# Optimization experiments

Hardware: AMD Instinct MI355X
Metric: run time of the kernel (lower is better)

## Reference

```python
import jax, jax.numpy as jnp
import numpy as np

NUM_EXPERTS = 64
TOP_K = 2
B, S, EMB, MLP = 4, 2048, 1024, 2048


def setup_inputs() -> dict:
    key = jax.random.key(0)
    k1, k2, k3, k4, k5 = jax.random.split(key, 5)
    inputs = jax.random.normal(k1, (B, S, EMB), dtype=jnp.float32)
    gate_kernel = jax.random.normal(k2, (EMB, NUM_EXPERTS), dtype=jnp.float32) / np.sqrt(EMB)
    w0 = jax.random.normal(k3, (NUM_EXPERTS, EMB, MLP), dtype=jnp.float32) / np.sqrt(EMB)
    w1 = jax.random.normal(k4, (NUM_EXPERTS, EMB, MLP), dtype=jnp.float32) / np.sqrt(EMB)
    wo = jax.random.normal(k5, (NUM_EXPERTS, MLP, EMB), dtype=jnp.float32) / np.sqrt(MLP)
    return {"inputs": inputs, "gate_kernel": gate_kernel, "w0": w0, "w1": w1, "wo": wo}


def reference(inputs, gate_kernel, w0, w1, wo):
    b, s, e = inputs.shape
    x = inputs.reshape(b * s, e)                                  # [T, E]
    # Router (DenseGeneral gate)
    gate_logits = jnp.einsum('te,ex->tx', x, gate_kernel)         # [T, X]
    # permute(): top-k gating + sort tokens by expert
    weights, selected = jax.lax.top_k(gate_logits, TOP_K)         # [T, K]
    weights = jax.nn.softmax(weights.astype(jnp.float32), axis=-1)
    flat_experts = selected.reshape(-1)                           # [T*K]
    sort_idx = jnp.argsort(flat_experts)                          # [T*K]
    token_idx = sort_idx // TOP_K
    sorted_x = jnp.take(x, token_idx, axis=0)                     # [T*K, E]
    group_sizes = jnp.bincount(flat_experts, length=NUM_EXPERTS).astype(jnp.int32)
    # grouped GEMMs (gated FFN: silu(x@w0) * (x@w1) @ wo)
    h0 = jax.lax.ragged_dot(sorted_x, w0, group_sizes)            # [T*K, M]
    h1 = jax.lax.ragged_dot(sorted_x, w1, group_sizes)            # [T*K, M]
    inter = jax.nn.silu(h0) * h1
    out_sorted = jax.lax.ragged_dot(inter, wo, group_sizes)       # [T*K, E]
    # unpermute(): restore token order, weighted combine over top-k
    unsorted = jnp.take(out_sorted, jnp.argsort(sort_idx), axis=0)
    per_tok = unsorted.reshape(b * s, TOP_K, e)
    out = jnp.einsum('BKE,BK->BE', per_tok.astype(jnp.float32), weights)
    return out.reshape(b, s, e)
```

## Files before the change

### kernel.cpp

```cpp
#include <hip/hip_runtime.h>
#include <hip/hip_bf16.h>
#include <math.h>

#define NTOK   8192
#define NEXP   64
#define EMBD   1024
#define MLPD   2048
#define TOPK   2
#define NFLAT  (NTOK * TOPK)
#define BKD    32
#define MAXCH  8

typedef __attribute__((ext_vector_type(4)))  float  f32x4;
typedef __attribute__((ext_vector_type(2)))  float  f32x2;
typedef __attribute__((ext_vector_type(16))) float  f32x16;
typedef __attribute__((ext_vector_type(8)))  __bf16 bf16x8;
typedef __attribute__((ext_vector_type(4)))  __bf16 bf16x4;

__device__ __forceinline__ void gl16(const void* g, void* lds_base) {
  __builtin_amdgcn_global_load_lds(
      (const __attribute__((address_space(1))) unsigned int*)g,
      (__attribute__((address_space(3))) unsigned int*)lds_base, 16, 0, 0);
}

#define OFF_COUNTS 0
#define OFF_BASE   256
#define OFF_RUN    512
#define OFF_EFLAT  1024
#define OFF_WFLAT  (1024 + 65536)
#define OFF_ROWTOK (1024 + 2 * 65536)
#define OFF_F2R    (1024 + 3 * 65536)
#define OFF_INTER  (1024 + 4 * 65536)
#define OFF_OS     (OFF_INTER + (size_t)NFLAT * MLPD * 2)
#define OFF_XB     OFF_OS
#define NEED_F32   (OFF_OS + (size_t)NFLAT * EMBD * 4)

__global__ __launch_bounds__(256) void cvt_x_k(const float* __restrict__ x,
                                               __bf16* __restrict__ xb) {
  size_t i = ((size_t)blockIdx.x * 256 + threadIdx.x) * 8;
  f32x4 f0 = *(const f32x4*)(x + i);
  f32x4 f1 = *(const f32x4*)(x + i + 4);
  bf16x8 v;
  #pragma unroll
  for (int q = 0; q < 4; ++q) { v[q] = (__bf16)f0[q]; v[4 + q] = (__bf16)f1[q]; }
  *(bf16x8*)(xb + i) = v;
}

__global__ __launch_bounds__(256) void router_topk(
    const float* __restrict__ x, const float* __restrict__ gk,
    int* __restrict__ e_flat, float* __restrict__ w_flat) {
  int t = blockIdx.x * 4 + (threadIdx.x >> 6);
  int l = threadIdx.x & 63;
  const float* xr = x + (size_t)t * EMBD;
  float acc = 0.f;
  #pragma unroll 8
  for (int i = 0; i < EMBD; ++i)
    acc = fmaf(xr[i], gk[i * NEXP + l], acc);
  float m = acc;
  for (int o = 32; o; o >>= 1) m = fmaxf(m, __shfl_xor(m, o));
  unsigned long long b1 = __ballot(acc == m);
  int i1 = __ffsll(b1) - 1;
  float v2 = (l == i1) ? -INFINITY : acc;
  float m2 = v2;
  for (int o = 32; o; o >>= 1) m2 = fmaxf(m2, __shfl_xor(m2, o));
  unsigned long long b2 = __ballot(v2 == m2);
  int i2 = __ffsll(b2) - 1;
  if (l == 0) {
    float e2 = expf(m2 - m);
    float inv = 1.f / (1.f + e2);
    e_flat[2 * t] = i1;  e_flat[2 * t + 1] = i2;
    w_flat[2 * t] = inv; w_flat[2 * t + 1] = e2 * inv;
  }
}

__global__ void hist_k(const int* __restrict__ ef, int* __restrict__ counts) {
  int j = blockIdx.x * 256 + threadIdx.x;
  if (j < NFLAT) atomicAdd(&counts[ef[j]], 1);
}

__global__ void scan_k(const int* __restrict__ counts, int* __restrict__ base) {
  if (threadIdx.x == 0) {
    int s = 0;
    for (int e = 0; e < NEXP; ++e) { base[e] = s; s += counts[e]; }
  }
}

__global__ void scatter_k(const int* __restrict__ ef, const int* __restrict__ base,
                          int* __restrict__ run, int* __restrict__ rowtok,
                          int* __restrict__ f2r) {
  int j = blockIdx.x * 256 + threadIdx.x;
  if (j < NFLAT) {
    int e = ef[j];
    int r = base[e] + atomicAdd(&run[e], 1);
    f2r[j] = r;
    rowtok[r] = j >> 1;
  }
}

__global__ __launch_bounds__(256, 3) void gemm1_k(
    const __bf16* __restrict__ xb, const float* __restrict__ w0,
    const float* __restrict__ w1, const int* __restrict__ counts,
    const int* __restrict__ base, const int* __restrict__ rowtok,
    __hip_bfloat16* __restrict__ inter) {
  int e = blockIdx.z;
  int Me = counts[e];
  int mc = blockIdx.y;
  if (mc * 128 >= Me) return;
  int rs = base[e];
  int nb = blockIdx.x * 64;
  int t = threadIdx.x;
  int wv = t >> 6, l = t & 63;
  int wr = wv >> 1, wc = wv & 1;
  int lo = l & 31, hi = l >> 5;

  __shared__ __bf16 Ax[3][4096];
  __shared__ __bf16 Bx[3][4096];

  int rga = mc * 128 + wv * 32 + lo; rga = rga < Me ? rga : Me - 1;
  const __bf16* abase = xb + (size_t)rowtok[rs + rga] * EMBD + hi * 8;
  int bm = t >> 7, ko = (t >> 5) & 3, np = t & 31;
  const float* bgb = (bm ? w1 : w0) + (size_t)e * EMBD * MLPD + nb + np * 2;
  int n0 = np * 2;
  int bslot = ((bm * 2 + (ko >> 1)) * 2 + (n0 >> 5)) * 64 + (ko & 1) * 32 + (n0 & 31);

  f32x2 vb[8];

  auto LOADB = [&](int ks) {
    int kk = ks * BKD;
    #pragma unroll
    for (int j = 0; j < 8; ++j)
      vb[j] = *(const f32x2*)(bgb + (size_t)(kk + ko * 8 + j) * MLPD);
  };
  auto WRITEB = [&](int buf) {
    bf16x8 c0, c1;
    #pragma unroll
    for (int j = 0; j < 8; ++j) { c0[j] = (__bf16)vb[j][0]; c1[j] = (__bf16)vb[j][1]; }
    *(bf16x8*)&Bx[buf][bslot * 8]     = c0;
    *(bf16x8*)&Bx[buf][bslot * 8 + 8] = c1;
  };
  auto STAGEA = [&](int ks, int buf) {
    int kk = ks * BKD;
    #pragma unroll
    for (int kh = 0; kh < 2; ++kh)
      gl16(abase + kk + kh * 16, &Ax[buf][(wv * 2 + kh) * 512]);
  };

  f32x16 acc0[2], acc1[2];
  #pragma unroll
  for (int g = 0; g < 2; ++g)
    #pragma unroll
    for (int r = 0; r < 16; ++r) { acc0[g][r] = 0.f; acc1[g][r] = 0.f; }

  const int NT = EMBD / BKD;
  LOADB(0);
  asm volatile("s_waitcnt vmcnt(0)" ::: "memory");
  WRITEB(0);
  LOADB(1);
  __builtin_amdgcn_sched_barrier(0);
  STAGEA(0, 0);
  STAGEA(1, 1);

  for (int ks = 0; ks < NT; ++ks) {
    int cur = ks % 3;
    if (ks + 1 < NT) asm volatile("s_waitcnt vmcnt(2)" ::: "memory");
    else             asm volatile("s_waitcnt vmcnt(0)" ::: "memory");
    __builtin_amdgcn_sched_barrier(0);
    asm volatile("s_waitcnt lgkmcnt(0)" ::: "memory");
    __builtin_amdgcn_sched_barrier(0);
    __builtin_amdgcn_s_barrier();
    if (ks + 1 < NT) WRITEB((ks + 1) % 3);
    __builtin_amdgcn_sched_barrier(0);
    if (ks + 2 < NT) LOADB(ks + 2);
    __builtin_amdgcn_sched_barrier(0);
    if (ks + 2 < NT) STAGEA(ks + 2, (ks + 2) % 3);
    __builtin_amdgcn_sched_barrier(0);

    bf16x8 av[2][2], bv0[2], bv1[2];
    #pragma unroll
    for (int g = 0; g < 2; ++g)
      #pragma unroll
      for (int kh = 0; kh < 2; ++kh)
        av[g][kh] = *(const bf16x8*)&Ax[cur][((wr * 2 + g) * 2 + kh) * 512 + l * 8];
    #pragma unroll
    for (int kh = 0; kh < 2; ++kh) {
      bv0[kh] = *(const bf16x8*)&Bx[cur][((0 + kh) * 2 + wc) * 512 + l * 8];
      bv1[kh] = *(const bf16x8*)&Bx[cur][((2 + kh) * 2 + wc) * 512 + l * 8];
    }
    #pragma unroll
    for (int kh = 0; kh < 2; ++kh)
      #pragma unroll
      for (int g = 0; g < 2; ++g) {
        acc0[g] = __builtin_amdgcn_mfma_f32_32x32x16_bf16(av[g][kh], bv0[kh], acc0[g], 0, 0, 0);
        acc1[g] = __builtin_amdgcn_mfma_f32_32x32x16_bf16(av[g][kh], bv1[kh], acc1[g], 0, 0, 0);
      }
  }

  #pragma unroll
  for (int g = 0; g < 2; ++g)
    #pragma unroll
    for (int r = 0; r < 16; ++r) {
      int rl = mc * 128 + wr * 64 + g * 32 + (r & 3) + 8 * (r >> 2) + 4 * hi;
      if (rl < Me) {
        float h0 = acc0[g][r], h1 = acc1[g][r];
        float s = h0 / (1.f + expf(-h0)) * h1;
        inter[(size_t)(rs + rl) * MLPD + nb + wc * 32 + lo] = (__hip_bfloat16)s;
      }
    }
}

template <typename OS_T>
__global__ __launch_bounds__(256, 4) void gemm2_k(
    const __hip_bfloat16* __restrict__ inter, const float* __restrict__ wo,
    const int* __restrict__ counts, const int* __restrict__ base,
    OS_T* __restrict__ os) {
  int e = blockIdx.z;
  int Me = counts[e];
  int mc = blockIdx.y;
  if (mc * 128 >= Me) return;
  int rs = base[e];
  int nb = blockIdx.x * 64;
  int t = threadIdx.x;
  int wv = t >> 6, l = t & 63;
  int wr = wv >> 1, wc = wv & 1;
  int lo = l & 31, hi = l >> 5;

  __shared__ __bf16 Ax[3][4096];
  __shared__ __bf16 Bx[3][2048];

  int rga = mc * 128 + wv * 32 + lo; rga = rga < Me ? rga : Me - 1;
  const __bf16* abase = (const __bf16*)inter + (size_t)(rs + rga) * MLPD + hi * 8;
  int kq = t >> 5, np = t & 31;
  const float* bgb = wo + (size_t)e * MLPD * EMBD + nb + np * 2;
  int n0 = np * 2;
  int bslot = ((kq >> 2) * 2 + (n0 >> 5)) * 64 + ((kq >> 1) & 1) * 32 + (n0 & 31);
  int qo = (kq & 1) * 4;

  f32x2 vb[4];

  auto LOADB = [&](int ks) {
    int kk = ks * BKD;
    #pragma unroll
    for (int j = 0; j < 4; ++j)
      vb[j] = *(const f32x2*)(bgb + (size_t)(kk + kq * 4 + j) * EMBD);
  };
  auto WRITEB = [&](int buf) {
    bf16x4 c0, c1;
    #pragma unroll
    for (int j = 0; j < 4; ++j) { c0[j] = (__bf16)vb[j][0]; c1[j] = (__bf16)vb[j][1]; }
    *(bf16x4*)&Bx[buf][bslot * 8 + qo]     = c0;
    *(bf16x4*)&Bx[buf][bslot * 8 + 8 + qo] = c1;
  };
  auto STAGEA = [&](int ks, int buf) {
    int kk = ks * BKD;
    #pragma unroll
    for (int kh = 0; kh < 2; ++kh)
      gl16(abase + kk + kh * 16, &Ax[buf][(wv * 2 + kh) * 512]);
  };

  f32x16 acc[2];
  #pragma unroll
  for (int g = 0; g < 2; ++g)
    #pragma unroll
    for (int r = 0; r < 16; ++r) acc[g][r] = 0.f;

  const int NT = MLPD / BKD;
  LOADB(0);
  asm volatile("s_waitcnt vmcnt(0)" ::: "memory");
  WRITEB(0);
  LOADB(1);
  __builtin_amdgcn_sched_barrier(0);
  STAGEA(0, 0);
  STAGEA(1, 1);

  for (int ks = 0; ks < NT; ++ks) {
    int cur = ks % 3;
    if (ks + 1 < NT) asm volatile("s_waitcnt vmcnt(2)" ::: "memory");
    else             asm volatile("s_waitcnt vmcnt(0)" ::: "memory");
    __builtin_amdgcn_sched_barrier(0);
    asm volatile("s_waitcnt lgkmcnt(0)" ::: "memory");
    __builtin_amdgcn_sched_barrier(0);
    __builtin_amdgcn_s_barrier();
    if (ks + 1 < NT) WRITEB((ks + 1) % 3);
    __builtin_amdgcn_sched_barrier(0);
    if (ks + 2 < NT) LOADB(ks + 2);
    __builtin_amdgcn_sched_barrier(0);
    if (ks + 2 < NT) STAGEA(ks + 2, (ks + 2) % 3);
    __builtin_amdgcn_sched_barrier(0);

    bf16x8 av[2][2], bv[2];
    #pragma unroll
    for (int g = 0; g < 2; ++g)
      #pragma unroll
      for (int kh = 0; kh < 2; ++kh)
        av[g][kh] = *(const bf16x8*)&Ax[cur][((wr * 2 + g) * 2 + kh) * 512 + l * 8];
    #pragma unroll
    for (int kh = 0; kh < 2; ++kh)
      bv[kh] = *(const bf16x8*)&Bx[cur][(kh * 2 + wc) * 512 + l * 8];
    #pragma unroll
    for (int kh = 0; kh < 2; ++kh)
      #pragma unroll
      for (int g = 0; g < 2; ++g)
        acc[g] = __builtin_amdgcn_mfma_f32_32x32x16_bf16(av[g][kh], bv[kh], acc[g], 0, 0, 0);
  }

  #pragma unroll
  for (int g = 0; g < 2; ++g)
    #pragma unroll
    for (int r = 0; r < 16; ++r) {
      int rl = mc * 128 + wr * 64 + g * 32 + (r & 3) + 8 * (r >> 2) + 4 * hi;
      if (rl < Me)
        os[(size_t)(rs + rl) * EMBD + nb + wc * 32 + lo] = (OS_T)acc[g][r];
    }
}

template <typename OS_T>
__global__ __launch_bounds__(256) void combine_k(
    const OS_T* __restrict__ os, const int* __restrict__ f2r,
    const float* __restrict__ wf, float* __restrict__ out) {
  int t = blockIdx.x;
  int c = threadIdx.x * 4;
  int r0 = f2r[2 * t], r1 = f2r[2 * t + 1];
  float wa = wf[2 * t], wb = wf[2 * t + 1];
  const OS_T* pa = os + (size_t)r0 * EMBD + c;
  const OS_T* pb = os + (size_t)r1 * EMBD + c;
  float4 o;
  o.x = wa * (float)pa[0] + wb * (float)pb[0];
  o.y = wa * (float)pa[1] + wb * (float)pb[1];
  o.z = wa * (float)pa[2] + wb * (float)pb[2];
  o.w = wa * (float)pa[3] + wb * (float)pb[3];
  *(float4*)(out + (size_t)t * EMBD + c) = o;
}

extern "C" void kernel_launch(void* const* d_in, const int* in_sizes, int n_in,
                              void* d_out, int out_size, void* d_ws, size_t ws_size,
                              hipStream_t stream) {
  const float* x  = (const float*)d_in[0];
  const float* gk = (const float*)d_in[1];
  const float* w0 = (const float*)d_in[2];
  const float* w1 = (const float*)d_in[3];
  const float* wo = (const float*)d_in[4];
  float* out = (float*)d_out;
  char* ws = (char*)d_ws;

  int*   counts = (int*)(ws + OFF_COUNTS);
  int*   basep  = (int*)(ws + OFF_BASE);
  int*   run    = (int*)(ws + OFF_RUN);
  int*   ef     = (int*)(ws + OFF_EFLAT);
  float* wfl    = (float*)(ws + OFF_WFLAT);
  int*   rowtok = (int*)(ws + OFF_ROWTOK);
  int*   f2r    = (int*)(ws + OFF_F2R);
  __hip_bfloat16* inter = (__hip_bfloat16*)(ws + OFF_INTER);
  __bf16* xb = (__bf16*)(ws + OFF_XB);

  hipMemsetAsync(ws, 0, 1024, stream);
  cvt_x_k<<<NTOK * EMBD / (256 * 8), 256, 0, stream>>>(x, xb);
  router_topk<<<NTOK / 4, 256, 0, stream>>>(x, gk, ef, wfl);
  hist_k<<<NFLAT / 256, 256, 0, stream>>>(ef, counts);
  scan_k<<<1, 64, 0, stream>>>(counts, basep);
  scatter_k<<<NFLAT / 256, 256, 0, stream>>>(ef, basep, run, rowtok, f2r);
  gemm1_k<<<dim3(MLPD / 64, MAXCH, NEXP), 256, 0, stream>>>(xb, w0, w1, counts, basep, rowtok, inter);

  if (ws_size >= NEED_F32) {
    float* os = (float*)(ws + OFF_OS);
    gemm2_k<float><<<dim3(EMBD / 64, MAXCH, NEXP), 256, 0, stream>>>(inter, wo, counts, basep, os);
    combine_k<float><<<NTOK, 256, 0, stream>>>(os, f2r, wfl, out);
  } else {
    __hip_bfloat16* os = (__hip_bfloat16*)(ws + OFF_OS);
    gemm2_k<__hip_bfloat16><<<dim3(EMBD / 64, MAXCH, NEXP), 256, 0, stream>>>(inter, wo, counts, basep, os);
    combine_k<__hip_bfloat16><<<NTOK, 256, 0, stream>>>(os, f2r, wfl, out);
  }
}
```

Before: 944.9 us.

## Deepen B-weight prefetch with double register sets, swizzle block-to-expert mapping, relayout B LDS

Both grouped GEMM kernels now keep two register sets of fp32 weight loads in flight, so B is prefetched three K-steps ahead instead of two. The loop is unrolled by two with rotating LDS buffer indices, and out-of-range loads are clamped instead of skipped, which keeps the vmcnt wait counts constant. Block indices are swizzled so that neighbouring blocks cover different experts and N tiles, spreading HBM traffic more evenly, and the B LDS layout changes to interleave columns. In exchange, register pressure rises and a few redundant loads are issued at the tail.

```diff
diff --git a/kernel.cpp b/kernel.cpp
--- a/kernel.cpp
+++ b/kernel.cpp
@@ -102,12 +102,14 @@
     const float* __restrict__ w1, const int* __restrict__ counts,
     const int* __restrict__ base, const int* __restrict__ rowtok,
     __hip_bfloat16* __restrict__ inter) {
-  int e = blockIdx.z;
+  int xr_ = blockIdx.x, zr_ = blockIdx.z;
+  int xi = (xr_ & ~7) | (zr_ & 7);
+  int e  = (zr_ & ~7) | (xr_ & 7);
   int Me = counts[e];
   int mc = blockIdx.y;
   if (mc * 128 >= Me) return;
   int rs = base[e];
-  int nb = blockIdx.x * 64;
+  int nb = xi * 64;
   int t = threadIdx.x;
   int wv = t >> 6, l = t & 63;
   int wr = wv >> 1, wc = wv & 1;
@@ -120,31 +122,10 @@
   const __bf16* abase = xb + (size_t)rowtok[rs + rga] * EMBD + hi * 8;
   int bm = t >> 7, ko = (t >> 5) & 3, np = t & 31;
   const float* bgb = (bm ? w1 : w0) + (size_t)e * EMBD * MLPD + nb + np * 2;
-  int n0 = np * 2;
-  int bslot = ((bm * 2 + (ko >> 1)) * 2 + (n0 >> 5)) * 64 + (ko & 1) * 32 + (n0 & 31);
-
-  f32x2 vb[8];
-
-  auto LOADB = [&](int ks) {
-    int kk = ks * BKD;
-    #pragma unroll
-    for (int j = 0; j < 8; ++j)
-      vb[j] = *(const f32x2*)(bgb + (size_t)(kk + ko * 8 + j) * MLPD);
-  };
-  auto WRITEB = [&](int buf) {
-    bf16x8 c0, c1;
-    #pragma unroll
-    for (int j = 0; j < 8; ++j) { c0[j] = (__bf16)vb[j][0]; c1[j] = (__bf16)vb[j][1]; }
-    *(bf16x8*)&Bx[buf][bslot * 8]     = c0;
-    *(bf16x8*)&Bx[buf][bslot * 8 + 8] = c1;
-  };
-  auto STAGEA = [&](int ks, int buf) {
-    int kk = ks * BKD;
-    #pragma unroll
-    for (int kh = 0; kh < 2; ++kh)
-      gl16(abase + kk + kh * 16, &Ax[buf][(wv * 2 + kh) * 512]);
-  };
-
+  int we0 = (((bm * 4 + ko) * 2 + 0) * 32 + np) * 8;
+  int we1 = (((bm * 4 + ko) * 2 + 1) * 32 + np) * 8;
+
+  f32x2 vbS0[8], vbS1[8];
   f32x16 acc0[2], acc1[2];
   #pragma unroll
   for (int g = 0; g < 2; ++g)
@@ -152,54 +133,86 @@
     for (int r = 0; r < 16; ++r) { acc0[g][r] = 0.f; acc1[g][r] = 0.f; }
 
   const int NT = EMBD / BKD;
-  LOADB(0);
+
+#define LOADB1(VB, KS)                                                     \
+  { int kkc = (KS) * BKD; kkc = kkc <= EMBD - BKD ? kkc : EMBD - BKD;      \
+    _Pragma("unroll")                                                      \
+    for (int q = 0; q < 8; ++q)                                            \
+      VB[q] = *(const f32x2*)(bgb + (size_t)(kkc + ko * 8 + q) * MLPD); }
+#define WRITEB1(VB, BUF)                                                   \
+  { bf16x8 c0_, c1_;                                                       \
+    _Pragma("unroll")                                                      \
+    for (int q = 0; q < 8; ++q) { c0_[q] = (__bf16)VB[q][0]; c1_[q] = (__bf16)VB[q][1]; } \
+    *(bf16x8*)&Bx[BUF][we0] = c0_;                                         \
+    *(bf16x8*)&Bx[BUF][we1] = c1_; }
+#define STAGEA1(KS, BUF)                                                   \
+  { int kkc = (KS) * BKD; kkc = kkc <= EMBD - BKD ? kkc : EMBD - BKD;      \
+    _Pragma("unroll")                                                      \
+    for (int kh = 0; kh < 2; ++kh)                                         \
+      gl16(abase + kkc + kh * 16, &Ax[BUF][(wv * 2 + kh) * 512]); }
+#define COMPUTE1(BUF)                                                      \
+  { bf16x8 av[2][2], bv0[2], bv1[2];                                       \
+    _Pragma("unroll")                                                      \
+    for (int g = 0; g < 2; ++g)                                            \
+      _Pragma("unroll")                                                    \
+      for (int kh = 0; kh < 2; ++kh)                                       \
+        av[g][kh] = *(const bf16x8*)&Ax[BUF][((wr * 2 + g) * 2 + kh) * 512 + l * 8]; \
+    _Pragma("unroll")                                                      \
+    for (int kh = 0; kh < 2; ++kh) {                                       \
+      int c_ = wc * 32 + lo;                                               \
+      bv0[kh] = *(const bf16x8*)&Bx[BUF][(((0 * 4 + kh * 2 + hi) * 2 + (c_ & 1)) * 32 + (c_ >> 1)) * 8]; \
+      bv1[kh] = *(const bf16x8*)&Bx[BUF][(((1 * 4 + kh * 2 + hi) * 2 + (c_ & 1)) * 32 + (c_ >> 1)) * 8]; \
+    }                                                                      \
+    _Pragma("unroll")                                                      \
+    for (int kh = 0; kh < 2; ++kh)                                         \
+      _Pragma("unroll")                                                    \
+      for (int g = 0; g < 2; ++g) {                                        \
+        acc0[g] = __builtin_amdgcn_mfma_f32_32x32x16_bf16(av[g][kh], bv0[kh], acc0[g], 0, 0, 0); \
+        acc1[g] = __builtin_amdgcn_mfma_f32_32x32x16_bf16(av[g][kh], bv1[kh], acc1[g], 0, 0, 0); \
+      } }
+#define G1_ITER(J, VB, bA, bB, bC)                                         \
+  { asm volatile("s_waitcnt vmcnt(10)" ::: "memory");                      \
+    asm volatile("s_waitcnt lgkmcnt(0)" ::: "memory");                     \
+    __builtin_amdgcn_sched_barrier(0);                                     \
+    __builtin_amdgcn_s_barrier();                                          \
+    if ((J) + 1 < NT) WRITEB1(VB, bB);                                     \
+    __builtin_amdgcn_sched_barrier(0);                                     \
+    LOADB1(VB, (J) + 3);                                                   \
+    __builtin_amdgcn_sched_barrier(0);                                     \
+    STAGEA1((J) + 2, bC);                                                  \
+    __builtin_amdgcn_sched_barrier(0);                                     \
+    COMPUTE1(bA); }
+
+  LOADB1(vbS0, 0);
   asm volatile("s_waitcnt vmcnt(0)" ::: "memory");
-  WRITEB(0);
-  LOADB(1);
-  __builtin_amdgcn_sched_barrier(0);
-  STAGEA(0, 0);
-  STAGEA(1, 1);
-
-  for (int ks = 0; ks < NT; ++ks) {
-    int cur = ks % 3;
-    if (ks + 1 < NT) asm volatile("s_waitcnt vmcnt(2)" ::: "memory");
-    else             asm volatile("s_waitcnt vmcnt(0)" ::: "memory");
-    __builtin_amdgcn_sched_barrier(0);
-    asm volatile("s_waitcnt lgkmcnt(0)" ::: "memory");
-    __builtin_amdgcn_sched_barrier(0);
-    __builtin_amdgcn_s_barrier();
-    if (ks + 1 < NT) WRITEB((ks + 1) % 3);
-    __builtin_amdgcn_sched_barrier(0);
-    if (ks + 2 < NT) LOADB(ks + 2);
-    __builtin_amdgcn_sched_barrier(0);
-    if (ks + 2 < NT) STAGEA(ks + 2, (ks + 2) % 3);
-    __builtin_amdgcn_sched_barrier(0);
-
-    bf16x8 av[2][2], bv0[2], bv1[2];
-    #pragma unroll
-    for (int g = 0; g < 2; ++g)
-      #pragma unroll
-      for (int kh = 0; kh < 2; ++kh)
-        av[g][kh] = *(const bf16x8*)&Ax[cur][((wr * 2 + g) * 2 + kh) * 512 + l * 8];
-    #pragma unroll
-    for (int kh = 0; kh < 2; ++kh) {
-      bv0[kh] = *(const bf16x8*)&Bx[cur][((0 + kh) * 2 + wc) * 512 + l * 8];
-      bv1[kh] = *(const bf16x8*)&Bx[cur][((2 + kh) * 2 + wc) * 512 + l * 8];
-    }
-    #pragma unroll
-    for (int kh = 0; kh < 2; ++kh)
-      #pragma unroll
-      for (int g = 0; g < 2; ++g) {
-        acc0[g] = __builtin_amdgcn_mfma_f32_32x32x16_bf16(av[g][kh], bv0[kh], acc0[g], 0, 0, 0);
-        acc1[g] = __builtin_amdgcn_mfma_f32_32x32x16_bf16(av[g][kh], bv1[kh], acc1[g], 0, 0, 0);
-      }
-  }
+  WRITEB1(vbS0, 0);
+  LOADB1(vbS1, 1);
+  __builtin_amdgcn_sched_barrier(0);
+  STAGEA1(0, 0);
+  __builtin_amdgcn_sched_barrier(0);
+  LOADB1(vbS0, 2);
+  __builtin_amdgcn_sched_barrier(0);
+  STAGEA1(1, 1);
+
+  int bA = 0, bB = 1, bC = 2;
+  for (int j = 0; j < NT; j += 2) {
+    G1_ITER(j, vbS1, bA, bB, bC);
+    { int tp = bA; bA = bB; bB = bC; bC = tp; }
+    G1_ITER(j + 1, vbS0, bA, bB, bC);
+    { int tp = bA; bA = bB; bB = bC; bC = tp; }
+  }
+  asm volatile("s_waitcnt vmcnt(0)" ::: "memory");
+#undef G1_ITER
+#undef COMPUTE1
+#undef STAGEA1
+#undef WRITEB1
+#undef LOADB1
 
   #pragma unroll
   for (int g = 0; g < 2; ++g)
     #pragma unroll
     for (int r = 0; r < 16; ++r) {
-      int rl = mc * 128 + wr * 64 + g * 32 + (r & 3) + 8 * (r >> 2) + 4 * hi;
+      int rl = mc * 128 + (wr * 2 + g) * 32 + (r & 3) + 8 * (r >> 2) + 4 * hi;
       if (rl < Me) {
         float h0 = acc0[g][r], h1 = acc1[g][r];
         float s = h0 / (1.f + expf(-h0)) * h1;
@@ -213,12 +226,14 @@
     const __hip_bfloat16* __restrict__ inter, const float* __restrict__ wo,
     const int* __restrict__ counts, const int* __restrict__ base,
     OS_T* __restrict__ os) {
-  int e = blockIdx.z;
+  int xr_ = blockIdx.x, zr_ = blockIdx.z;
+  int xi = (xr_ & 8) | (zr_ & 7);
+  int e  = (zr_ & ~7) | (xr_ & 7);
   int Me = counts[e];
   int mc = blockIdx.y;
   if (mc * 128 >= Me) return;
   int rs = base[e];
-  int nb = blockIdx.x * 64;
+  int nb = xi * 64;
   int t = threadIdx.x;
   int wv = t >> 6, l = t & 63;
   int wr = wv >> 1, wc = wv & 1;
@@ -231,32 +246,11 @@
   const __bf16* abase = (const __bf16*)inter + (size_t)(rs + rga) * MLPD + hi * 8;
   int kq = t >> 5, np = t & 31;
   const float* bgb = wo + (size_t)e * MLPD * EMBD + nb + np * 2;
-  int n0 = np * 2;
-  int bslot = ((kq >> 2) * 2 + (n0 >> 5)) * 64 + ((kq >> 1) & 1) * 32 + (n0 & 31);
-  int qo = (kq & 1) * 4;
-
-  f32x2 vb[4];
-
-  auto LOADB = [&](int ks) {
-    int kk = ks * BKD;
-    #pragma unroll
-    for (int j = 0; j < 4; ++j)
-      vb[j] = *(const f32x2*)(bgb + (size_t)(kk + kq * 4 + j) * EMBD);
-  };
-  auto WRITEB = [&](int buf) {
-    bf16x4 c0, c1;
-    #pragma unroll
-    for (int j = 0; j < 4; ++j) { c0[j] = (__bf16)vb[j][0]; c1[j] = (__bf16)vb[j][1]; }
-    *(bf16x4*)&Bx[buf][bslot * 8 + qo]     = c0;
-    *(bf16x4*)&Bx[buf][bslot * 8 + 8 + qo] = c1;
-  };
-  auto STAGEA = [&](int ks, int buf) {
-    int kk = ks * BKD;
-    #pragma unroll
-    for (int kh = 0; kh < 2; ++kh)
-      gl16(abase + kk + kh * 16, &Ax[buf][(wv * 2 + kh) * 512]);
-  };
-
+  int o_ = kq >> 1, h2 = kq & 1;
+  int we0 = ((o_ * 2 + 0) * 32 + np) * 8 + h2 * 4;
+  int we1 = ((o_ * 2 + 1) * 32 + np) * 8 + h2 * 4;
+
+  f32x2 vbS0[4], vbS1[4];
   f32x16 acc[2];
   #pragma unroll
   for (int g = 0; g < 2; ++g)
@@ -264,50 +258,83 @@
     for (int r = 0; r < 16; ++r) acc[g][r] = 0.f;
 
   const int NT = MLPD / BKD;
-  LOADB(0);
+
+#define LOADB2(VB, KS)                                                     \
+  { int kkc = (KS) * BKD; kkc = kkc <= MLPD - BKD ? kkc : MLPD - BKD;      \
+    _Pragma("unroll")                                                      \
+    for (int q = 0; q < 4; ++q)                                            \
+      VB[q] = *(const f32x2*)(bgb + (size_t)(kkc + kq * 4 + q) * EMBD); }
+#define WRITEB2(VB, BUF)                                                   \
+  { bf16x4 c0_, c1_;                                                       \
+    _Pragma("unroll")                                                      \
+    for (int q = 0; q < 4; ++q) { c0_[q] = (__bf16)VB[q][0]; c1_[q] = (__bf16)VB[q][1]; } \
+    *(bf16x4*)&Bx[BUF][we0] = c0_;                                         \
+    *(bf16x4*)&Bx[BUF][we1] = c1_; }
+#define STAGEA2(KS, BUF)                                                   \
+  { int kkc = (KS) * BKD; kkc = kkc <= MLPD - BKD ? kkc : MLPD - BKD;      \
+    _Pragma("unroll")                                                      \
+    for (int kh = 0; kh < 2; ++kh)                                         \
+      gl16(abase + kkc + kh * 16, &Ax[BUF][(wv * 2 + kh) * 512]); }
+#define COMPUTE2(BUF)                                                      \
+  { bf16x8 av[2][2], bv[2];                                                \
+    _Pragma("unroll")                                                      \
+    for (int g = 0; g < 2; ++g)                                            \
+      _Pragma("unroll")                                                    \
+      for (int kh = 0; kh < 2; ++kh)                                       \
+        av[g][kh] = *(const bf16x8*)&Ax[BUF][((wr * 2 + g) * 2 + kh) * 512 + l * 8]; \
+    _Pragma("unroll")                                                      \
+    for (int kh = 0; kh < 2; ++kh) {                                       \
+      int c_ = wc * 32 + lo;                                               \
+      bv[kh] = *(const bf16x8*)&Bx[BUF][(((kh * 2 + hi) * 2 + (c_ & 1)) * 32 + (c_ >> 1)) * 8]; \
+    }                                                                      \
+    _Pragma("unroll")                                                      \
+    for (int kh = 0; kh < 2; ++kh)                                         \
+      _Pragma("unroll")                                                    \
+      for (int g = 0; g < 2; ++g)                                          \
+        acc[g] = __builtin_amdgcn_mfma_f32_32x32x16_bf16(av[g][kh], bv[kh], acc[g], 0, 0, 0); }
+#define G2_ITER(J, VB, bA, bB, bC)                                         \
+  { asm volatile("s_waitcnt vmcnt(6)" ::: "memory");                       \
+    asm volatile("s_waitcnt lgkmcnt(0)" ::: "memory");                     \
+    __builtin_amdgcn_sched_barrier(0);                                     \
+    __builtin_amdgcn_s_barrier();                                          \
+    if ((J) + 1 < NT) WRITEB2(VB, bB);                                     \
+    __builtin_amdgcn_sched_barrier(0);                                     \
+    LOADB2(VB, (J) + 3);                                                   \
+    __builtin_amdgcn_sched_barrier(0);                                     \
+    STAGEA2((J) + 2, bC);                                                  \
+    __builtin_amdgcn_sched_barrier(0);                                     \
+    COMPUTE2(bA); }
+
+  LOADB2(vbS0, 0);
   asm volatile("s_waitcnt vmcnt(0)" ::: "memory");
-  WRITEB(0);
-  LOADB(1);
-  __builtin_amdgcn_sched_barrier(0);
-  STAGEA(0, 0);
-  STAGEA(1, 1);
-
-  for (int ks = 0; ks < NT; ++ks) {
-    int cur = ks % 3;
-    if (ks + 1 < NT) asm volatile("s_waitcnt vmcnt(2)" ::: "memory");
-    else             asm volatile("s_waitcnt vmcnt(0)" ::: "memory");
-    __builtin_amdgcn_sched_barrier(0);
-    asm volatile("s_waitcnt lgkmcnt(0)" ::: "memory");
-    __builtin_amdgcn_sched_barrier(0);
-    __builtin_amdgcn_s_barrier();
-    if (ks + 1 < NT) WRITEB((ks + 1) % 3);
-    __builtin_amdgcn_sched_barrier(0);
-    if (ks + 2 < NT) LOADB(ks + 2);
-    __builtin_amdgcn_sched_barrier(0);
-    if (ks + 2 < NT) STAGEA(ks + 2, (ks + 2) % 3);
-    __builtin_amdgcn_sched_barrier(0);
-
-    bf16x8 av[2][2], bv[2];
-    #pragma unroll
-    for (int g = 0; g < 2; ++g)
-      #pragma unroll
-      for (int kh = 0; kh < 2; ++kh)
-        av[g][kh] = *(const bf16x8*)&Ax[cur][((wr * 2 + g) * 2 + kh) * 512 + l * 8];
-    #pragma unroll
-    for (int kh = 0; kh < 2; ++kh)
-      bv[kh] = *(const bf16x8*)&Bx[cur][(kh * 2 + wc) * 512 + l * 8];
-    #pragma unroll
-    for (int kh = 0; kh < 2; ++kh)
-      #pragma unroll
-      for (int g = 0; g < 2; ++g)
-        acc[g] = __builtin_amdgcn_mfma_f32_32x32x16_bf16(av[g][kh], bv[kh], acc[g], 0, 0, 0);
-  }
+  WRITEB2(vbS0, 0);
+  LOADB2(vbS1, 1);
+  __builtin_amdgcn_sched_barrier(0);
+  STAGEA2(0, 0);
+  __builtin_amdgcn_sched_barrier(0);
+  LOADB2(vbS0, 2);
+  __builtin_amdgcn_sched_barrier(0);
+  STAGEA2(1, 1);
+
+  int bA = 0, bB = 1, bC = 2;
+  for (int j = 0; j < NT; j += 2) {
+    G2_ITER(j, vbS1, bA, bB, bC);
+    { int tp = bA; bA = bB; bB = bC; bC = tp; }
+    G2_ITER(j + 1, vbS0, bA, bB, bC);
+    { int tp = bA; bA = bB; bB = bC; bC = tp; }
+  }
+  asm volatile("s_waitcnt vmcnt(0)" ::: "memory");
+#undef G2_ITER
+#undef COMPUTE2
+#undef STAGEA2
+#undef WRITEB2
+#undef LOADB2
 
   #pragma unroll
   for (int g = 0; g < 2; ++g)
     #pragma unroll
     for (int r = 0; r < 16; ++r) {
-      int rl = mc * 128 + wr * 64 + g * 32 + (r & 3) + 8 * (r >> 2) + 4 * hi;
+      int rl = mc * 128 + (wr * 2 + g) * 32 + (r & 3) + 8 * (r >> 2) + 4 * hi;
       if (rl < Me)
         os[(size_t)(rs + rl) * EMBD + nb + wc * 32 + lo] = (OS_T)acc[g][r];
     }
```

Measured after the change: 1.027 ms. 1.09x slower.

## Fuse weighted combine into gemm2 via atomic adds and stage fp32 wo with direct-to-LDS loads

Applied to the files above, without the earlier changes.

The separate combine kernel and the intermediate per-row output buffer are removed. gemm2 now scales each row by its routing weight and atomically adds into the zeroed output at the token's position. The wo tile is also staged as fp32 straight into LDS with global_load_lds and converted to bf16 at fragment-read time, replacing the register load/convert/write path. This trades the extra round trip through the output buffer for float atomics, a memset of the output, larger LDS use (occupancy hint lowered to 3), and scalar strided LDS reads for B.

```diff
diff --git a/kernel.cpp b/kernel.cpp
--- a/kernel.cpp
+++ b/kernel.cpp
@@ -15,7 +15,6 @@
 typedef __attribute__((ext_vector_type(2)))  float  f32x2;
 typedef __attribute__((ext_vector_type(16))) float  f32x16;
 typedef __attribute__((ext_vector_type(8)))  __bf16 bf16x8;
-typedef __attribute__((ext_vector_type(4)))  __bf16 bf16x4;
 
 __device__ __forceinline__ void gl16(const void* g, void* lds_base) {
   __builtin_amdgcn_global_load_lds(
@@ -29,11 +28,9 @@
 #define OFF_EFLAT  1024
 #define OFF_WFLAT  (1024 + 65536)
 #define OFF_ROWTOK (1024 + 2 * 65536)
-#define OFF_F2R    (1024 + 3 * 65536)
+#define OFF_ROWWT  (1024 + 3 * 65536)
 #define OFF_INTER  (1024 + 4 * 65536)
-#define OFF_OS     (OFF_INTER + (size_t)NFLAT * MLPD * 2)
-#define OFF_XB     OFF_OS
-#define NEED_F32   (OFF_OS + (size_t)NFLAT * EMBD * 4)
+#define OFF_XB     (OFF_INTER + (size_t)NFLAT * MLPD * 2)
 
 __global__ __launch_bounds__(256) void cvt_x_k(const float* __restrict__ x,
                                                __bf16* __restrict__ xb) {
@@ -85,15 +82,15 @@
   }
 }
 
-__global__ void scatter_k(const int* __restrict__ ef, const int* __restrict__ base,
-                          int* __restrict__ run, int* __restrict__ rowtok,
-                          int* __restrict__ f2r) {
+__global__ void scatter_k(const int* __restrict__ ef, const float* __restrict__ wf,
+                          const int* __restrict__ base, int* __restrict__ run,
+                          int* __restrict__ rowtok, float* __restrict__ rowwt) {
   int j = blockIdx.x * 256 + threadIdx.x;
   if (j < NFLAT) {
     int e = ef[j];
     int r = base[e] + atomicAdd(&run[e], 1);
-    f2r[j] = r;
     rowtok[r] = j >> 1;
+    rowwt[r] = wf[j];
   }
 }
 
@@ -199,7 +196,7 @@
   for (int g = 0; g < 2; ++g)
     #pragma unroll
     for (int r = 0; r < 16; ++r) {
-      int rl = mc * 128 + wr * 64 + g * 32 + (r & 3) + 8 * (r >> 2) + 4 * hi;
+      int rl = mc * 128 + (wr * 2 + g) * 32 + (r & 3) + 8 * (r >> 2) + 4 * hi;
       if (rl < Me) {
         float h0 = acc0[g][r], h1 = acc1[g][r];
         float s = h0 / (1.f + expf(-h0)) * h1;
@@ -208,11 +205,11 @@
     }
 }
 
-template <typename OS_T>
-__global__ __launch_bounds__(256, 4) void gemm2_k(
+__global__ __launch_bounds__(256, 3) void gemm2_k(
     const __hip_bfloat16* __restrict__ inter, const float* __restrict__ wo,
     const int* __restrict__ counts, const int* __restrict__ base,
-    OS_T* __restrict__ os) {
+    const int* __restrict__ rowtok, const float* __restrict__ rowwt,
+    float* __restrict__ out) {
   int e = blockIdx.z;
   int Me = counts[e];
   int mc = blockIdx.y;
@@ -224,38 +221,24 @@
   int wr = wv >> 1, wc = wv & 1;
   int lo = l & 31, hi = l >> 5;
 
-  __shared__ __bf16 Ax[3][4096];
-  __shared__ __bf16 Bx[3][2048];
+  __shared__ __bf16 A2[3][4096];
+  __shared__ float  B2[3][2048];
 
   int rga = mc * 128 + wv * 32 + lo; rga = rga < Me ? rga : Me - 1;
   const __bf16* abase = (const __bf16*)inter + (size_t)(rs + rga) * MLPD + hi * 8;
-  int kq = t >> 5, np = t & 31;
-  const float* bgb = wo + (size_t)e * MLPD * EMBD + nb + np * 2;
-  int n0 = np * 2;
-  int bslot = ((kq >> 2) * 2 + (n0 >> 5)) * 64 + ((kq >> 1) & 1) * 32 + (n0 & 31);
-  int qo = (kq & 1) * 4;
-
-  f32x2 vb[4];
-
-  auto LOADB = [&](int ks) {
+  const float* wbase = wo + (size_t)e * MLPD * EMBD + nb + (l & 15) * 4 +
+                       (size_t)(l >> 4) * EMBD;
+
+  auto STAGE = [&](int ks, int buf) {
     int kk = ks * BKD;
     #pragma unroll
-    for (int j = 0; j < 4; ++j)
-      vb[j] = *(const f32x2*)(bgb + (size_t)(kk + kq * 4 + j) * EMBD);
+    for (int kh = 0; kh < 2; ++kh)
+      gl16(abase + kk + kh * 16, &A2[buf][(wv * 2 + kh) * 512]);
+    #pragma unroll
+    for (int j = 0; j < 2; ++j)
+      gl16(wbase + (size_t)(kk + wv * 8 + j * 4) * EMBD,
+           &B2[buf][(wv * 8 + j * 4) * 64]);
   };
-  auto WRITEB = [&](int buf) {
-    bf16x4 c0, c1;
-    #pragma unroll
-    for (int j = 0; j < 4; ++j) { c0[j] = (__bf16)vb[j][0]; c1[j] = (__bf16)vb[j][1]; }
-    *(bf16x4*)&Bx[buf][bslot * 8 + qo]     = c0;
-    *(bf16x4*)&Bx[buf][bslot * 8 + 8 + qo] = c1;
-  };
-  auto STAGEA = [&](int ks, int buf) {
-    int kk = ks * BKD;
-    #pragma unroll
-    for (int kh = 0; kh < 2; ++kh)
-      gl16(abase + kk + kh * 16, &Ax[buf][(wv * 2 + kh) * 512]);
-  };
 
   f32x16 acc[2];
   #pragma unroll
@@ -264,71 +247,55 @@
     for (int r = 0; r < 16; ++r) acc[g][r] = 0.f;
 
   const int NT = MLPD / BKD;
-  LOADB(0);
-  asm volatile("s_waitcnt vmcnt(0)" ::: "memory");
-  WRITEB(0);
-  LOADB(1);
-  __builtin_amdgcn_sched_barrier(0);
-  STAGEA(0, 0);
-  STAGEA(1, 1);
-
+  STAGE(0, 0);
+  STAGE(1, 1);
+  int bufR = 0, bufW = 2;
   for (int ks = 0; ks < NT; ++ks) {
-    int cur = ks % 3;
-    if (ks + 1 < NT) asm volatile("s_waitcnt vmcnt(2)" ::: "memory");
+    if (ks + 1 < NT) asm volatile("s_waitcnt vmcnt(4)" ::: "memory");
     else             asm volatile("s_waitcnt vmcnt(0)" ::: "memory");
     __builtin_amdgcn_sched_barrier(0);
-    asm volatile("s_waitcnt lgkmcnt(0)" ::: "memory");
-    __builtin_amdgcn_sched_barrier(0);
     __builtin_amdgcn_s_barrier();
-    if (ks + 1 < NT) WRITEB((ks + 1) % 3);
-    __builtin_amdgcn_sched_barrier(0);
-    if (ks + 2 < NT) LOADB(ks + 2);
-    __builtin_amdgcn_sched_barrier(0);
-    if (ks + 2 < NT) STAGEA(ks + 2, (ks + 2) % 3);
-    __builtin_amdgcn_sched_barrier(0);
-
-    bf16x8 av[2][2], bv[2];
+    if (ks + 2 < NT) STAGE(ks + 2, bufW);
+
+    bf16x8 av[2][2];
     #pragma unroll
     for (int g = 0; g < 2; ++g)
       #pragma unroll
       for (int kh = 0; kh < 2; ++kh)
-        av[g][kh] = *(const bf16x8*)&Ax[cur][((wr * 2 + g) * 2 + kh) * 512 + l * 8];
-    #pragma unroll
-    for (int kh = 0; kh < 2; ++kh)
-      bv[kh] = *(const bf16x8*)&Bx[cur][(kh * 2 + wc) * 512 + l * 8];
+        av[g][kh] = *(const bf16x8*)&A2[bufR][((wr * 2 + g) * 2 + kh) * 512 + l * 8];
+    float b[2][8];
+    #pragma unroll
+    for (int kh = 0; kh < 2; ++kh) {
+      int bi = (kh * 16 + hi * 8) * 64 + wc * 32 + lo;
+      #pragma unroll
+      for (int q = 0; q < 8; ++q) b[kh][q] = B2[bufR][bi + q * 64];
+    }
+    bf16x8 bv[2];
+    #pragma unroll
+    for (int kh = 0; kh < 2; ++kh)
+      #pragma unroll
+      for (int q = 0; q < 8; ++q) bv[kh][q] = (__bf16)b[kh][q];
     #pragma unroll
     for (int kh = 0; kh < 2; ++kh)
       #pragma unroll
       for (int g = 0; g < 2; ++g)
         acc[g] = __builtin_amdgcn_mfma_f32_32x32x16_bf16(av[g][kh], bv[kh], acc[g], 0, 0, 0);
+    bufR = bufR == 2 ? 0 : bufR + 1;
+    bufW = bufW == 2 ? 0 : bufW + 1;
   }
 
   #pragma unroll
   for (int g = 0; g < 2; ++g)
     #pragma unroll
     for (int r = 0; r < 16; ++r) {
-      int rl = mc * 128 + wr * 64 + g * 32 + (r & 3) + 8 * (r >> 2) + 4 * hi;
-      if (rl < Me)
-        os[(size_t)(rs + rl) * EMBD + nb + wc * 32 + lo] = (OS_T)acc[g][r];
+      int rl = mc * 128 + (wr * 2 + g) * 32 + (r & 3) + 8 * (r >> 2) + 4 * hi;
+      if (rl < Me) {
+        int row = rs + rl;
+        float wt = rowwt[row];
+        atomicAdd(&out[(size_t)rowtok[row] * EMBD + nb + wc * 32 + lo],
+                  wt * acc[g][r]);
+      }
     }
-}
-
-template <typename OS_T>
-__global__ __launch_bounds__(256) void combine_k(
-    const OS_T* __restrict__ os, const int* __restrict__ f2r,
-    const float* __restrict__ wf, float* __restrict__ out) {
-  int t = blockIdx.x;
-  int c = threadIdx.x * 4;
-  int r0 = f2r[2 * t], r1 = f2r[2 * t + 1];
-  float wa = wf[2 * t], wb = wf[2 * t + 1];
-  const OS_T* pa = os + (size_t)r0 * EMBD + c;
-  const OS_T* pb = os + (size_t)r1 * EMBD + c;
-  float4 o;
-  o.x = wa * (float)pa[0] + wb * (float)pb[0];
-  o.y = wa * (float)pa[1] + wb * (float)pb[1];
-  o.z = wa * (float)pa[2] + wb * (float)pb[2];
-  o.w = wa * (float)pa[3] + wb * (float)pb[3];
-  *(float4*)(out + (size_t)t * EMBD + c) = o;
 }
 
 extern "C" void kernel_launch(void* const* d_in, const int* in_sizes, int n_in,
@@ -348,25 +315,17 @@
   int*   ef     = (int*)(ws + OFF_EFLAT);
   float* wfl    = (float*)(ws + OFF_WFLAT);
   int*   rowtok = (int*)(ws + OFF_ROWTOK);
-  int*   f2r    = (int*)(ws + OFF_F2R);
+  float* rowwt  = (float*)(ws + OFF_ROWWT);
   __hip_bfloat16* inter = (__hip_bfloat16*)(ws + OFF_INTER);
   __bf16* xb = (__bf16*)(ws + OFF_XB);
 
   hipMemsetAsync(ws, 0, 1024, stream);
+  hipMemsetAsync(out, 0, (size_t)NTOK * EMBD * 4, stream);
   cvt_x_k<<<NTOK * EMBD / (256 * 8), 256, 0, stream>>>(x, xb);
   router_topk<<<NTOK / 4, 256, 0, stream>>>(x, gk, ef, wfl);
   hist_k<<<NFLAT / 256, 256, 0, stream>>>(ef, counts);
   scan_k<<<1, 64, 0, stream>>>(counts, basep);
-  scatter_k<<<NFLAT / 256, 256, 0, stream>>>(ef, basep, run, rowtok, f2r);
+  scatter_k<<<NFLAT / 256, 256, 0, stream>>>(ef, wfl, basep, run, rowtok, rowwt);
   gemm1_k<<<dim3(MLPD / 64, MAXCH, NEXP), 256, 0, stream>>>(xb, w0, w1, counts, basep, rowtok, inter);
-
-  if (ws_size >= NEED_F32) {
-    float* os = (float*)(ws + OFF_OS);
-    gemm2_k<float><<<dim3(EMBD / 64, MAXCH, NEXP), 256, 0, stream>>>(inter, wo, counts, basep, os);
-    combine_k<float><<<NTOK, 256, 0, stream>>>(os, f2r, wfl, out);
-  } else {
-    __hip_bfloat16* os = (__hip_bfloat16*)(ws + OFF_OS);
-    gemm2_k<__hip_bfloat16><<<dim3(EMBD / 64, MAXCH, NEXP), 256, 0, stream>>>(inter, wo, counts, basep, os);
-    combine_k<__hip_bfloat16><<<NTOK, 256, 0, stream>>>(os, f2r, wfl, out);
-  }
-}
+  gemm2_k<<<dim3(EMBD / 64, MAXCH, NEXP), 256, 0, stream>>>(inter, wo, counts, basep, rowtok, rowwt, out);
+}
```

Result: no change. 963.6 us (+2.0%).
